# Kernel optimization log

Hardware: AMD Instinct MI355X
Metric: run time of the kernel (lower is better)

## Reference

```python
import jax, jax.numpy as jnp
import numpy as np

N_NODES = 150000
N_EDGES = 4800000
IN_DIM, HID_DIM, OUT_DIM = 1433, 16, 7


def setup_inputs() -> dict:
    key = jax.random.key(0)
    ks = jax.random.split(key, 8)
    features = jax.random.normal(ks[0], (N_NODES, IN_DIM), dtype=jnp.float32)
    edge_src = jax.random.randint(ks[1], (N_EDGES,), 0, N_NODES, dtype=jnp.int32)
    edge_dst = jax.random.randint(ks[2], (N_EDGES,), 0, N_NODES, dtype=jnp.int32)
    adj_vals = jax.random.uniform(ks[3], (N_EDGES,), dtype=jnp.float32)
    W1 = jax.random.normal(ks[4], (IN_DIM, HID_DIM), dtype=jnp.float32) * (1.0 / np.sqrt(IN_DIM))
    b1 = jnp.zeros((HID_DIM,), dtype=jnp.float32)
    W2 = jax.random.normal(ks[5], (HID_DIM, OUT_DIM), dtype=jnp.float32) * (1.0 / np.sqrt(HID_DIM))
    b2 = jnp.zeros((OUT_DIM,), dtype=jnp.float32)
    return {"features": features, "edge_src": edge_src, "edge_dst": edge_dst,
            "adj_vals": adj_vals, "W1": W1, "b1": b1, "W2": W2, "b2": b2}


def _gcn_layer(x, edge_src, edge_dst, adj_vals, W, b):
    # h = A_hat @ (x @ W) + b ; dense transform first since in_dim >= out_dim
    xw = x @ W                                   # [N, d_out]
    msg = adj_vals[:, None] * xw[edge_src]       # [E, d_out] gather
    agg = jax.ops.segment_sum(msg, edge_dst, num_segments=x.shape[0])  # scatter-add
    return agg + b


def reference(features, edge_src, edge_dst, adj_vals, W1, b1, W2, b2):
    h1 = jax.nn.relu(_gcn_layer(features, edge_src, edge_dst, adj_vals, W1, b1))
    # dropout in original forward is a no-op (result discarded) -> omitted
    h2 = _gcn_layer(h1, edge_src, edge_dst, adj_vals, W2, b2)
    return jax.nn.log_softmax(h2, axis=1)
```

## Files before the change

kernel.cpp:

```cpp
#include <hip/hip_runtime.h>
#include <float.h>
#include <stdint.h>

#define IN_DIM 1433
#define HID 16
#define OUTD 7

#define KC 32
#define GROWS 64
#define NT 45
#define KLAST 25

#define AS1 __attribute__((address_space(1)))
#define AS3 __attribute__((address_space(3)))

__global__ __launch_bounds__(256, 8) void gemm1_kernel(
    const float* __restrict__ feat, const float* __restrict__ W1,
    float* __restrict__ xw1, int N)
{
    __shared__ float xs[2][GROWS * KC];
    const int t = threadIdx.x;
    const int lane = t & 63;
    const int w = t >> 6;
    const int row0 = blockIdx.x * GROWS;
    const long maxElem = (long)N * IN_DIM - 1;

    const int r  = t & 63;
    const int rb = r & 7;
    const int q4 = __builtin_amdgcn_readfirstlane(w) * 4;

    float acc[4] = {0.f, 0.f, 0.f, 0.f};

    auto stage = [&](int buf, int k0) {
#pragma unroll
        for (int i = 0; i < 8; ++i) {
            const int ri = (i * 4 + w) * 2 + (lane >> 5);
            const int cs = lane & 31;
            const int gcol = (cs & 3) | (((cs >> 2) ^ (ri & 7)) << 2);
            long elem = (long)(row0 + ri) * IN_DIM + k0 + gcol;
            if (elem > maxElem) elem = maxElem;
            __builtin_amdgcn_global_load_lds(
                (const AS1 void*)(feat + elem),
                (AS3 void*)(&xs[buf][(i * 4 + w) * 64]), 4, 0, 0);
        }
    };

#define COMPUTE(buf, k0v, KMAX)                                              \
    {                                                                        \
        const float* xrow = &xs[buf][r * KC];                                \
        _Pragma("unroll")                                                    \
        for (int b = 0; b < ((KMAX) >> 2); ++b) {                            \
            const float4 xv = *(const float4*)&xrow[((b ^ rb) << 2)];        \
            const float* wk = W1 + (size_t)((k0v) + 4 * b) * HID + q4;       \
            const float4 w0 = *(const float4*)(wk);                          \
            const float4 w1 = *(const float4*)(wk + HID);                    \
            const float4 w2 = *(const float4*)(wk + 2 * HID);                \
            const float4 w3 = *(const float4*)(wk + 3 * HID);                \
            acc[0] += xv.x * w0.x; acc[1] += xv.x * w0.y;                    \
            acc[2] += xv.x * w0.z; acc[3] += xv.x * w0.w;                    \
            acc[0] += xv.y * w1.x; acc[1] += xv.y * w1.y;                    \
            acc[2] += xv.y * w1.z; acc[3] += xv.y * w1.w;                    \
            acc[0] += xv.z * w2.x; acc[1] += xv.z * w2.y;                    \
            acc[2] += xv.z * w2.z; acc[3] += xv.z * w2.w;                    \
            acc[0] += xv.w * w3.x; acc[1] += xv.w * w3.y;                    \
            acc[2] += xv.w * w3.z; acc[3] += xv.w * w3.w;                    \
        }                                                                    \
        if ((KMAX) & 3) {                     \
            const int b = (KMAX) >> 2;                                       \
            const float4 xv = *(const float4*)&xrow[((b ^ rb) << 2)];        \
            const float* wk = W1 + (size_t)((k0v) + 4 * b) * HID + q4;       \
            const float4 w0 = *(const float4*)(wk);                          \
            acc[0] += xv.x * w0.x; acc[1] += xv.x * w0.y;                    \
            acc[2] += xv.x * w0.z; acc[3] += xv.x * w0.w;                    \
        }                                                                    \
    }

    stage(0, 0);
    __syncthreads();
    for (int it = 0; it < NT - 1; ++it) {
        stage((it & 1) ^ 1, (it + 1) * KC);
        COMPUTE(it & 1, it * KC, KC);
        __syncthreads();
    }
    COMPUTE((NT - 1) & 1, (NT - 1) * KC, KLAST);
#undef COMPUTE

    const int grow = row0 + r;
    if (grow < N)
        *(float4*)(xw1 + (size_t)grow * HID + q4) =
            make_float4(acc[0], acc[1], acc[2], acc[3]);
}

__global__ __launch_bounds__(256) void hist_kernel(
    const int* __restrict__ dst, int* __restrict__ cnt, int E)
{
    const int i4 = blockIdx.x * 256 + threadIdx.x;
    const int e0 = i4 * 4;
    if (e0 + 3 < E) {
        const int4 d = ((const int4*)dst)[i4];
        atomicAdd(&cnt[d.x], 1);
        atomicAdd(&cnt[d.y], 1);
        atomicAdd(&cnt[d.z], 1);
        atomicAdd(&cnt[d.w], 1);
    } else {
        for (int e = e0; e < E; ++e) atomicAdd(&cnt[dst[e]], 1);
    }
}

__global__ __launch_bounds__(256) void scan1_kernel(
    const int* __restrict__ cnt, int* __restrict__ offs,
    int* __restrict__ bsum, int N)
{
    __shared__ int lds[256];
    const int t = threadIdx.x, b = blockIdx.x;
    const int base = b * 1024 + t * 4;
    int c0 = 0, c1 = 0, c2 = 0, c3 = 0;
    if (base + 0 < N) c0 = cnt[base + 0];
    if (base + 1 < N) c1 = cnt[base + 1];
    if (base + 2 < N) c2 = cnt[base + 2];
    if (base + 3 < N) c3 = cnt[base + 3];
    const int s = c0 + c1 + c2 + c3;
    lds[t] = s;
    __syncthreads();
    for (int off = 1; off < 256; off <<= 1) {
        int v = (t >= off) ? lds[t - off] : 0;
        __syncthreads();
        lds[t] += v;
        __syncthreads();
    }
    const int excl = lds[t] - s;
    if (t == 255) bsum[b] = lds[255];
    int run = excl;
    if (base + 0 < N) { offs[base + 0] = run; run += c0; }
    if (base + 1 < N) { offs[base + 1] = run; run += c1; }
    if (base + 2 < N) { offs[base + 2] = run; run += c2; }
    if (base + 3 < N) { offs[base + 3] = run; run += c3; }
}

__global__ __launch_bounds__(256) void scan2_kernel(
    const int* __restrict__ bsum, int* __restrict__ bbase, int NB)
{
    __shared__ int lds[256];
    const int t = threadIdx.x;
    const int v = (t < NB) ? bsum[t] : 0;
    lds[t] = v;
    __syncthreads();
    for (int off = 1; off < 256; off <<= 1) {
        int u = (t >= off) ? lds[t - off] : 0;
        __syncthreads();
        lds[t] += u;
        __syncthreads();
    }
    bbase[t] = lds[t] - v;
}

__global__ __launch_bounds__(256) void scan3_kernel(
    int* __restrict__ offs, int* __restrict__ cursor,
    const int* __restrict__ bbase, int N, int E)
{
    const int t = threadIdx.x, b = blockIdx.x;
    const int add = bbase[b];
    const int base = b * 1024 + t * 4;
#pragma unroll
    for (int i = 0; i < 4; ++i) {
        const int idx = base + i;
        if (idx < N) {
            const int v = offs[idx] + add;
            offs[idx] = v;
            cursor[idx] = v;
        }
    }
    if (b == 0 && t == 0) offs[N] = E;
}

__global__ __launch_bounds__(256) void fill_kernel(
    const int* __restrict__ src, const int* __restrict__ dst,
    const float* __restrict__ a, int* __restrict__ cursor,
    uint2* __restrict__ pairs, int E)
{
    const int i4 = blockIdx.x * 256 + threadIdx.x;
    const int e0 = i4 * 4;
    if (e0 + 3 < E) {
        const int4   s4 = ((const int4*)src)[i4];
        const int4   d4 = ((const int4*)dst)[i4];
        const float4 a4 = ((const float4*)a)[i4];
        int p0 = atomicAdd(&cursor[d4.x], 1);
        pairs[p0] = make_uint2((unsigned)s4.x, __float_as_uint(a4.x));
        int p1 = atomicAdd(&cursor[d4.y], 1);
        pairs[p1] = make_uint2((unsigned)s4.y, __float_as_uint(a4.y));
        int p2 = atomicAdd(&cursor[d4.z], 1);
        pairs[p2] = make_uint2((unsigned)s4.z, __float_as_uint(a4.z));
        int p3 = atomicAdd(&cursor[d4.w], 1);
        pairs[p3] = make_uint2((unsigned)s4.w, __float_as_uint(a4.w));
    } else {
        for (int e = e0; e < E; ++e) {
            const int pos = atomicAdd(&cursor[dst[e]], 1);
            pairs[pos] = make_uint2((unsigned)src[e], __float_as_uint(a[e]));
        }
    }
}

__global__ __launch_bounds__(256) void gather1_kernel(
    const uint2* __restrict__ pairs, const int* __restrict__ offs,
    const float* __restrict__ xw1, const float* __restrict__ b1,
    const float* __restrict__ W2, float* __restrict__ xw2, int N)
{
    __shared__ float w2s[HID * OUTD];
    const int t = threadIdx.x;
    if (t < HID * OUTD) w2s[t] = W2[t];
    __syncthreads();
    const int lane = t & 63;
    const int r = blockIdx.x * 4 + (t >> 6);
    if (r >= N) return;
    const int g = lane >> 2;
    const int c = lane & 3;
    const int start = offs[r], end = offs[r + 1];
    float4 acc = make_float4(0.f, 0.f, 0.f, 0.f);
    int e = start + g;
    for (; e + 16 < end; e += 32) {
        const uint2 p0 = pairs[e];
        const uint2 p1 = pairs[e + 16];
        const float4 v0 = *(const float4*)(xw1 + (size_t)p0.x * HID + c * 4);
        const float4 v1 = *(const float4*)(xw1 + (size_t)p1.x * HID + c * 4);
        const float a0 = __uint_as_float(p0.y);
        const float a1 = __uint_as_float(p1.y);
        acc.x += a0 * v0.x + a1 * v1.x;
        acc.y += a0 * v0.y + a1 * v1.y;
        acc.z += a0 * v0.z + a1 * v1.z;
        acc.w += a0 * v0.w + a1 * v1.w;
    }
    if (e < end) {
        const uint2 p0 = pairs[e];
        const float4 v0 = *(const float4*)(xw1 + (size_t)p0.x * HID + c * 4);
        const float a0 = __uint_as_float(p0.y);
        acc.x += a0 * v0.x; acc.y += a0 * v0.y;
        acc.z += a0 * v0.z; acc.w += a0 * v0.w;
    }
#pragma unroll
    for (int m = 4; m < 64; m <<= 1) {
        acc.x += __shfl_xor(acc.x, m);
        acc.y += __shfl_xor(acc.y, m);
        acc.z += __shfl_xor(acc.z, m);
        acc.w += __shfl_xor(acc.w, m);
    }
    const float4 b1v = ((const float4*)b1)[c];
    float4 hv;
    hv.x = fmaxf(acc.x + b1v.x, 0.f);
    hv.y = fmaxf(acc.y + b1v.y, 0.f);
    hv.z = fmaxf(acc.z + b1v.z, 0.f);
    hv.w = fmaxf(acc.w + b1v.w, 0.f);
    float hh[16];
#pragma unroll
    for (int cc = 0; cc < 4; ++cc) {
        hh[cc * 4 + 0] = __shfl(hv.x, cc);
        hh[cc * 4 + 1] = __shfl(hv.y, cc);
        hh[cc * 4 + 2] = __shfl(hv.z, cc);
        hh[cc * 4 + 3] = __shfl(hv.w, cc);
    }
    const int col = (lane & 7) < OUTD ? (lane & 7) : 0;
    float sacc = 0.f;
#pragma unroll
    for (int j = 0; j < HID; ++j) sacc += hh[j] * w2s[j * OUTD + col];
    if (lane < 8) xw2[(size_t)r * 8 + lane] = (lane < OUTD) ? sacc : 0.f;
}

__global__ __launch_bounds__(256) void gather2_kernel(
    const uint2* __restrict__ pairs, const int* __restrict__ offs,
    const float* __restrict__ xw2, const float* __restrict__ b2,
    float* __restrict__ out, int N)
{
    const int t = threadIdx.x;
    const int lane = t & 63;
    const int r = blockIdx.x * 4 + (t >> 6);
    if (r >= N) return;
    const int g = lane >> 1;
    const int c = lane & 1;
    const int start = offs[r], end = offs[r + 1];
    float4 acc = make_float4(0.f, 0.f, 0.f, 0.f);
    for (int e = start + g; e < end; e += 32) {
        const uint2 p = pairs[e];
        const float4 v = *(const float4*)(xw2 + (size_t)p.x * 8 + c * 4);
        const float a = __uint_as_float(p.y);
        acc.x += a * v.x; acc.y += a * v.y;
        acc.z += a * v.z; acc.w += a * v.w;
    }
#pragma unroll
    for (int m = 2; m < 64; m <<= 1) {
        acc.x += __shfl_xor(acc.x, m);
        acc.y += __shfl_xor(acc.y, m);
        acc.z += __shfl_xor(acc.z, m);
        acc.w += __shfl_xor(acc.w, m);
    }
    float4 x;
    if (c == 0) {
        const float4 b2v = *(const float4*)b2;
        x.x = acc.x + b2v.x; x.y = acc.y + b2v.y;
        x.z = acc.z + b2v.z; x.w = acc.w + b2v.w;
    } else {
        x.x = acc.x + b2[4]; x.y = acc.y + b2[5];
        x.z = acc.z + b2[6]; x.w = -FLT_MAX;
    }
    float mymax = fmaxf(fmaxf(x.x, x.y), x.z);
    if (c == 0) mymax = fmaxf(mymax, x.w);
    const float m = fmaxf(mymax, __shfl_xor(mymax, 1));
    float es = expf(x.x - m) + expf(x.y - m) + expf(x.z - m);
    if (c == 0) es += expf(x.w - m);
    const float s = es + __shfl_xor(es, 1);
    const float lg = logf(s);
    float* op = out + (size_t)r * OUTD;
    if (c == 0) {
        op[0] = x.x - m - lg; op[1] = x.y - m - lg;
        op[2] = x.z - m - lg; op[3] = x.w - m - lg;
    } else {
        op[4] = x.x - m - lg; op[5] = x.y - m - lg;
        op[6] = x.z - m - lg;
    }
}

extern "C" void kernel_launch(void* const* d_in, const int* in_sizes, int n_in,
                              void* d_out, int out_size, void* d_ws, size_t ws_size,
                              hipStream_t stream)
{
    const float* feat  = (const float*)d_in[0];
    const int*   esrc  = (const int*)d_in[1];
    const int*   edst  = (const int*)d_in[2];
    const float* avals = (const float*)d_in[3];
    const float* W1    = (const float*)d_in[4];
    const float* b1    = (const float*)d_in[5];
    const float* W2    = (const float*)d_in[6];
    const float* b2    = (const float*)d_in[7];
    float* out = (float*)d_out;

    const int N = in_sizes[0] / IN_DIM;
    const int E = in_sizes[1];
    const int NB = (N + 1023) / 1024;

    char* p = (char*)d_ws;
    float* xw1   = (float*)p; p += (size_t)N * HID * sizeof(float);
    float* xw2   = (float*)p; p += (size_t)N * 8 * sizeof(float);
    int*   cnt   = (int*)p;   p += (size_t)N * sizeof(int);
    int*   offs  = (int*)p;   p += (size_t)(N + 1) * sizeof(int);
    int*   cursor= (int*)p;   p += (size_t)N * sizeof(int);
    int*   bsum  = (int*)p;   p += 256 * sizeof(int);
    int*   bbase = (int*)p;   p += 256 * sizeof(int);
    p = (char*)(((uintptr_t)p + 15) & ~(uintptr_t)15);
    uint2* pairs = (uint2*)p;

    hipMemsetAsync(cnt, 0, (size_t)N * sizeof(int), stream);

    gemm1_kernel<<<(N + GROWS - 1) / GROWS, 256, 0, stream>>>(feat, W1, xw1, N);

    {
        const int n4 = (E + 3) / 4;
        hist_kernel<<<(n4 + 255) / 256, 256, 0, stream>>>(edst, cnt, E);
    }
    scan1_kernel<<<NB, 256, 0, stream>>>(cnt, offs, bsum, N);
    scan2_kernel<<<1, 256, 0, stream>>>(bsum, bbase, NB);
    scan3_kernel<<<NB, 256, 0, stream>>>(offs, cursor, bbase, N, E);
    {
        const int n4 = (E + 3) / 4;
        fill_kernel<<<(n4 + 255) / 256, 256, 0, stream>>>(esrc, edst, avals, cursor, pairs, E);
    }

    gather1_kernel<<<(N + 3) / 4, 256, 0, stream>>>(pairs, offs, xw1, b1, W2, xw2, N);
    gather2_kernel<<<(N + 3) / 4, 256, 0, stream>>>(pairs, offs, xw2, b2, out, N);
}
```

Baseline: 1.001 ms.

## Restructure GEMM1 to per-wave 16-byte LDS staging with full 16-wide accumulators

Rewrites the feature×W1 kernel so each thread computes all 16 output columns for one row, with each wave staging its own rows using 16-byte global_load_lds and aligning each row to a 16-float boundary through a per-wave scalar prefix. Block-wide __syncthreads is replaced by per-wave vmcnt waits over a double buffer, and blocks now cover 256 rows. The aim is wider loads, no redundant X reads across four column groups, and no block barriers, at the cost of more registers (occupancy hint lowered to 4) and more complex, hardcoded tail handling.

After: 954.6 us (median of 2 runs). 4.7% less time.

```diff
diff --git a/kernel.cpp b/kernel.cpp
--- a/kernel.cpp
+++ b/kernel.cpp
@@ -6,89 +6,130 @@
 #define HID 16
 #define OUTD 7
 
-#define KC 32
-#define GROWS 64
-#define NT 45
-#define KLAST 25
-
 #define AS1 __attribute__((address_space(1)))
 #define AS3 __attribute__((address_space(3)))
 
-__global__ __launch_bounds__(256, 8) void gemm1_kernel(
+__global__ __launch_bounds__(256, 4) void gemm1_kernel(
     const float* __restrict__ feat, const float* __restrict__ W1,
     float* __restrict__ xw1, int N)
 {
-    __shared__ float xs[2][GROWS * KC];
+    __shared__ float xs[4][2][64 * 16];
     const int t = threadIdx.x;
-    const int lane = t & 63;
+    const int l = t & 63;
     const int w = t >> 6;
-    const int row0 = blockIdx.x * GROWS;
-    const long maxElem = (long)N * IN_DIM - 1;
-
-    const int r  = t & 63;
-    const int rb = r & 7;
-    const int q4 = __builtin_amdgcn_readfirstlane(w) * 4;
-
-    float acc[4] = {0.f, 0.f, 0.f, 0.f};
-
-    auto stage = [&](int buf, int k0) {
-#pragma unroll
-        for (int i = 0; i < 8; ++i) {
-            const int ri = (i * 4 + w) * 2 + (lane >> 5);
-            const int cs = lane & 31;
-            const int gcol = (cs & 3) | (((cs >> 2) ^ (ri & 7)) << 2);
-            long elem = (long)(row0 + ri) * IN_DIM + k0 + gcol;
-            if (elem > maxElem) elem = maxElem;
+    const int row0 = blockIdx.x * 256;
+    const int h = __builtin_amdgcn_readfirstlane((4 - w) & 3);
+    const long maxBase = (long)N * IN_DIM - 4;
+
+    const int R = row0 + 4 * l + w;
+
+    long src[4];
+#pragma unroll
+    for (int j = 0; j < 4; ++j) {
+        const int rc = j * 16 + (l >> 2);
+        const int bs = (l & 3) ^ (rc & 3);
+        src[j] = (long)(row0 + 4 * rc + w) * IN_DIM + h + 4 * bs;
+    }
+
+    float acc[16];
+#pragma unroll
+    for (int j = 0; j < 16; ++j) acc[j] = 0.f;
+
+    for (int k = 0; k < h; ++k) {
+        const float x = (R < N) ? feat[(long)R * IN_DIM + k] : 0.f;
+        const float* wr = W1 + k * HID;
+#pragma unroll
+        for (int j = 0; j < 16; ++j) acc[j] += x * wr[j];
+    }
+    asm volatile("s_waitcnt vmcnt(0)" ::: "memory");
+    __builtin_amdgcn_sched_barrier(0);
+
+    auto stage = [&](int buf, int i) {
+#pragma unroll
+        for (int j = 0; j < 4; ++j) {
+            long e = src[j] + 16 * i;
+            if (e > maxBase) e = maxBase;
             __builtin_amdgcn_global_load_lds(
-                (const AS1 void*)(feat + elem),
-                (AS3 void*)(&xs[buf][(i * 4 + w) * 64]), 4, 0, 0);
+                (const AS1 void*)(feat + e),
+                (AS3 void*)(&xs[w][buf][j * 256]), 16, 0, 0);
         }
     };
 
-#define COMPUTE(buf, k0v, KMAX)                                              \
+#define WAITVM(Nimm)                                                         \
+    asm volatile("s_waitcnt vmcnt(" #Nimm ")" ::: "memory");                 \
+    __builtin_amdgcn_sched_barrier(0);
+
+    const int lx = l & 3;
+#define COMPUTE_FULL(buf, i)                                                 \
     {                                                                        \
-        const float* xrow = &xs[buf][r * KC];                                \
+        const float* xrow = &xs[w][buf][l * 16];                             \
+        const int kb0 = h + 16 * (i);                                        \
         _Pragma("unroll")                                                    \
-        for (int b = 0; b < ((KMAX) >> 2); ++b) {                            \
-            const float4 xv = *(const float4*)&xrow[((b ^ rb) << 2)];        \
-            const float* wk = W1 + (size_t)((k0v) + 4 * b) * HID + q4;       \
-            const float4 w0 = *(const float4*)(wk);                          \
-            const float4 w1 = *(const float4*)(wk + HID);                    \
-            const float4 w2 = *(const float4*)(wk + 2 * HID);                \
-            const float4 w3 = *(const float4*)(wk + 3 * HID);                \
-            acc[0] += xv.x * w0.x; acc[1] += xv.x * w0.y;                    \
-            acc[2] += xv.x * w0.z; acc[3] += xv.x * w0.w;                    \
-            acc[0] += xv.y * w1.x; acc[1] += xv.y * w1.y;                    \
-            acc[2] += xv.y * w1.z; acc[3] += xv.y * w1.w;                    \
-            acc[0] += xv.z * w2.x; acc[1] += xv.z * w2.y;                    \
-            acc[2] += xv.z * w2.z; acc[3] += xv.z * w2.w;                    \
-            acc[0] += xv.w * w3.x; acc[1] += xv.w * w3.y;                    \
-            acc[2] += xv.w * w3.z; acc[3] += xv.w * w3.w;                    \
+        for (int b = 0; b < 4; ++b) {                                        \
+            const float4 xv = *(const float4*)&xrow[((b ^ lx) << 2)];        \
+            const float* wk = W1 + (size_t)(kb0 + 4 * b) * HID;              \
+            _Pragma("unroll")                                                \
+            for (int e = 0; e < 4; ++e) {                                    \
+                const float xe = ((const float*)&xv)[e];                     \
+                const float4 wA = *(const float4*)(wk + e * HID);            \
+                const float4 wB = *(const float4*)(wk + e * HID + 4);        \
+                const float4 wC = *(const float4*)(wk + e * HID + 8);        \
+                const float4 wD = *(const float4*)(wk + e * HID + 12);       \
+                acc[0]  += xe * wA.x; acc[1]  += xe * wA.y;                  \
+                acc[2]  += xe * wA.z; acc[3]  += xe * wA.w;                  \
+                acc[4]  += xe * wB.x; acc[5]  += xe * wB.y;                  \
+                acc[6]  += xe * wB.z; acc[7]  += xe * wB.w;                  \
+                acc[8]  += xe * wC.x; acc[9]  += xe * wC.y;                  \
+                acc[10] += xe * wC.z; acc[11] += xe * wC.w;                  \
+                acc[12] += xe * wD.x; acc[13] += xe * wD.y;                  \
+                acc[14] += xe * wD.z; acc[15] += xe * wD.w;                  \
+            }                                                                \
         }                                                                    \
-        if ((KMAX) & 3) {                     \
-            const int b = (KMAX) >> 2;                                       \
-            const float4 xv = *(const float4*)&xrow[((b ^ rb) << 2)];        \
-            const float* wk = W1 + (size_t)((k0v) + 4 * b) * HID + q4;       \
-            const float4 w0 = *(const float4*)(wk);                          \
-            acc[0] += xv.x * w0.x; acc[1] += xv.x * w0.y;                    \
-            acc[2] += xv.x * w0.z; acc[3] += xv.x * w0.w;                    \
-        }                                                                    \
     }
 
     stage(0, 0);
-    __syncthreads();
-    for (int it = 0; it < NT - 1; ++it) {
-        stage((it & 1) ^ 1, (it + 1) * KC);
-        COMPUTE(it & 1, it * KC, KC);
-        __syncthreads();
-    }
-    COMPUTE((NT - 1) & 1, (NT - 1) * KC, KLAST);
-#undef COMPUTE
-
-    const int grow = row0 + r;
-    if (grow < N)
-        *(float4*)(xw1 + (size_t)grow * HID + q4) =
-            make_float4(acc[0], acc[1], acc[2], acc[3]);
+    stage(1, 1);
+    for (int i = 0; i < 88; ++i) {
+        WAITVM(4);
+        COMPUTE_FULL(i & 1, i);
+        stage(i & 1, i + 2);
+    }
+    WAITVM(4);
+    COMPUTE_FULL(0, 88);
+    WAITVM(0);
+    {
+        const int kl = 9 - h;
+        const int nb = kl >> 2, tl = kl & 3;
+        const float* xrow = &xs[w][1][l * 16];
+        const int kb0 = h + 16 * 89;
+        for (int b = 0; b < nb; ++b) {
+            const float4 xv = *(const float4*)&xrow[((b ^ lx) << 2)];
+            const float* wk = W1 + (size_t)(kb0 + 4 * b) * HID;
+#pragma unroll
+            for (int e = 0; e < 4; ++e) {
+                const float xe = ((const float*)&xv)[e];
+                const float* wr = wk + e * HID;
+#pragma unroll
+                for (int j = 0; j < 16; ++j) acc[j] += xe * wr[j];
+            }
+        }
+        for (int kk = nb * 4; kk < nb * 4 + tl; ++kk) {
+            const float x = xrow[(((kk >> 2) ^ lx) << 2) | (kk & 3)];
+            const float* wr = W1 + (size_t)(kb0 + kk) * HID;
+#pragma unroll
+            for (int j = 0; j < 16; ++j) acc[j] += x * wr[j];
+        }
+    }
+#undef COMPUTE_FULL
+#undef WAITVM
+
+    if (R < N) {
+        float4* o = (float4*)(xw1 + (size_t)R * HID);
+        o[0] = make_float4(acc[0],  acc[1],  acc[2],  acc[3]);
+        o[1] = make_float4(acc[4],  acc[5],  acc[6],  acc[7]);
+        o[2] = make_float4(acc[8],  acc[9],  acc[10], acc[11]);
+        o[3] = make_float4(acc[12], acc[13], acc[14], acc[15]);
+    }
 }
 
 __global__ __launch_bounds__(256) void hist_kernel(
@@ -348,7 +389,7 @@
 
     hipMemsetAsync(cnt, 0, (size_t)N * sizeof(int), stream);
 
-    gemm1_kernel<<<(N + GROWS - 1) / GROWS, 256, 0, stream>>>(feat, W1, xw1, N);
+    gemm1_kernel<<<(N + 255) / 256, 256, 0, stream>>>(feat, W1, xw1, N);
 
     {
         const int n4 = (E + 3) / 4;
```
